# Performance work log

Measured on AMD Instinct MI355X. Metric: run time of the kernel, lower is better.

## Reference

```python
import jax, jax.numpy as jnp
import numpy as np

D_MODEL = 256
NUM_HEADS = 8
NUM_KV_HEADS = 4
HEAD_DIM = D_MODEL // NUM_HEADS
EPS = 1e-5


def layer_norm(x, g, b):
    mu = jnp.mean(x, axis=-1, keepdims=True)
    var = jnp.var(x, axis=-1, keepdims=True)
    return (x - mu) * jax.lax.rsqrt(var + EPS) * g + b


def gqa(x_q, x_kv, Wq, bq, Wk, bk, Wv, bv, Wo, bo):
    # x_q, x_kv: [BC, S, D]
    BC, S, D = x_q.shape
    G = NUM_HEADS // NUM_KV_HEADS
    q = (x_q @ Wq + bq).reshape(BC, S, NUM_HEADS, HEAD_DIM)
    k = (x_kv @ Wk + bk).reshape(BC, S, NUM_KV_HEADS, HEAD_DIM)
    v = (x_kv @ Wv + bv).reshape(BC, S, NUM_KV_HEADS, HEAD_DIM)
    # repeat_interleave over head dim to expand KV heads to query heads
    k = jnp.repeat(k, G, axis=2)
    v = jnp.repeat(v, G, axis=2)
    scale = 1.0 / np.sqrt(HEAD_DIM).astype(np.float32)
    scores = jnp.einsum('bqhd,bkhd->bhqk', q, k) * scale  # [BC,H,S,S]
    attn = jax.nn.softmax(scores, axis=-1)
    out = jnp.einsum('bhqk,bkhd->bqhd', attn, v).reshape(BC, S, D)
    return out @ Wo + bo


def _make_params(key):
    ks = jax.random.split(key, 20)
    D, Dkv = D_MODEL, NUM_KV_HEADS * HEAD_DIM
    s = 1.0 / np.sqrt(D).astype(np.float32)
    p = {}
    # 4 LayerNorms
    for name in ['spec_q', 'spec_kv', 'spat_q', 'spat_kv']:
        p[f'ln_{name}_g'] = jnp.ones((D,), jnp.float32)
        p[f'ln_{name}_b'] = jnp.zeros((D,), jnp.float32)
    # two GQA modules: s2t and t2s
    i = 0
    for tag in ['s2t', 't2s']:
        p[f'Wq_{tag}'] = jax.random.normal(ks[i], (D, D), jnp.float32) * s; i += 1
        p[f'bq_{tag}'] = jnp.zeros((D,), jnp.float32)
        p[f'Wk_{tag}'] = jax.random.normal(ks[i], (D, Dkv), jnp.float32) * s; i += 1
        p[f'bk_{tag}'] = jnp.zeros((Dkv,), jnp.float32)
        p[f'Wv_{tag}'] = jax.random.normal(ks[i], (D, Dkv), jnp.float32) * s; i += 1
        p[f'bv_{tag}'] = jnp.zeros((Dkv,), jnp.float32)
        p[f'Wo_{tag}'] = jax.random.normal(ks[i], (D, D), jnp.float32) * s; i += 1
        p[f'bo_{tag}'] = jnp.zeros((D,), jnp.float32)
    p['gate_spec'] = jnp.zeros((1,), jnp.float32)
    p['gate_spat'] = jnp.zeros((1,), jnp.float32)
    return p


def setup_inputs() -> dict:
    key = jax.random.key(0)
    k1, k2, k3 = jax.random.split(key, 3)
    B, S, C, D = 8, 64, 128, D_MODEL
    inp = {
        'x_spec': jax.random.normal(k1, (B, S, C, D), jnp.float32),
        'x_spat': jax.random.normal(k2, (B, S, C, D), jnp.float32),
    }
    inp.update(_make_params(k3))
    return inp


def reference(x_spec, x_spat,
              ln_spec_q_g, ln_spec_q_b, ln_spec_kv_g, ln_spec_kv_b,
              ln_spat_q_g, ln_spat_q_b, ln_spat_kv_g, ln_spat_kv_b,
              Wq_s2t, bq_s2t, Wk_s2t, bk_s2t, Wv_s2t, bv_s2t, Wo_s2t, bo_s2t,
              Wq_t2s, bq_t2s, Wk_t2s, bk_t2s, Wv_t2s, bv_t2s, Wo_t2s, bo_t2s,
              gate_spec, gate_spat):
    B, S, C, D = x_spec.shape
    # (B,S,C,D) -> (B*C, S, D)
    spec_flat = jnp.transpose(x_spec, (0, 2, 1, 3)).reshape(B * C, S, D)
    spat_flat = jnp.transpose(x_spat, (0, 2, 1, 3)).reshape(B * C, S, D)

    spec_q = layer_norm(spec_flat, ln_spec_q_g, ln_spec_q_b)
    spat_kv = layer_norm(spat_flat, ln_spat_kv_g, ln_spat_kv_b)
    delta_spec = gqa(spec_q, spat_kv, Wq_s2t, bq_s2t, Wk_s2t, bk_s2t, Wv_s2t, bv_s2t, Wo_s2t, bo_s2t)

    spat_q = layer_norm(spat_flat, ln_spat_q_g, ln_spat_q_b)
    spec_kv = layer_norm(spec_flat, ln_spec_kv_g, ln_spec_kv_b)
    delta_spat = gqa(spat_q, spec_kv, Wq_t2s, bq_t2s, Wk_t2s, bk_t2s, Wv_t2s, bv_t2s, Wo_t2s, bo_t2s)

    delta_spec = jnp.transpose(delta_spec.reshape(B, C, S, D), (0, 2, 1, 3))
    delta_spat = jnp.transpose(delta_spat.reshape(B, C, S, D), (0, 2, 1, 3))

    out_spec = x_spec + jax.nn.sigmoid(gate_spec) * delta_spec
    out_spat = x_spat + jax.nn.sigmoid(gate_spat) * delta_spat
    return (out_spec, out_spat)
```

## Files before the change

kernel.cpp:

```cpp
#include <hip/hip_runtime.h>

typedef short short8 __attribute__((ext_vector_type(8)));
typedef float f32x4 __attribute__((ext_vector_type(4)));

#define NELT 16777216

__device__ __forceinline__ float b2f(unsigned short u) {
    return __uint_as_float(((unsigned)u) << 16);
}
__device__ __forceinline__ unsigned short f2b(float f) {
    unsigned u = __float_as_uint(f);
    u += 0x7FFF + ((u >> 16) & 1);
    return (unsigned short)(u >> 16);
}
__device__ __forceinline__ void split2(float f, unsigned short& hi, unsigned short& lo) {
    unsigned short h = f2b(f);
    hi = h;
    lo = f2b(f - b2f(h));
}
__device__ __forceinline__ int xrow_off(int r) {
    int n = r >> 6, s = r & 63;
    int b = n >> 7, c = n & 127;
    return (((b << 6) + s) * 128 + c) << 8;
}
__device__ __forceinline__ int sw256(int row, int k) {
    return row * 256 + ((((k >> 3) ^ (row & 7)) << 3) | (k & 7));
}
__device__ __forceinline__ int boff(int nt, int kk, int ct, int lq, int lm) {
    return ((((nt * 8 + kk) * 4 + ct) * 4 + lq) * 16 + lm) * 16;
}

struct WArgs {
    const float* Wq[2]; const float* Wk[2]; const float* Wv[2]; const float* Wo[2];
    unsigned short* Bqkv[2]; unsigned short* Bo[2];
};
__global__ __launch_bounds__(256) void w_prep(WArgs A)
{
    const int dir = blockIdx.y;
    const int tid = blockIdx.x * 256 + threadIdx.x;
    const int lm = tid & 15, lq = (tid >> 4) & 3, ct = (tid >> 6) & 3;
    const int kk = (tid >> 8) & 7, nt = tid >> 11;
    const int c = ct * 16 + lm;
    {
        const float* W; int ldw, col;
        if (nt < 4)      { W = A.Wq[dir]; ldw = 256; col = nt * 64 + c; }
        else if (nt < 6) { W = A.Wk[dir]; ldw = 128; col = (nt - 4) * 64 + c; }
        else             { W = A.Wv[dir]; ldw = 128; col = (nt - 6) * 64 + c; }
        short8 h8, l8;
        #pragma unroll
        for (int j = 0; j < 8; ++j) {
            int k = kk * 32 + lq * 8 + j;
            unsigned short h, l;
            split2(W[k * ldw + col], h, l);
            h8[j] = (short)h; l8[j] = (short)l;
        }
        int off = boff(nt, kk, ct, lq, lm);
        *(short8*)&A.Bqkv[dir][off] = h8;
        *(short8*)&A.Bqkv[dir][off + 8] = l8;
    }
    if (nt < 4) {
        int col = nt * 64 + c;
        short8 h8, l8;
        #pragma unroll
        for (int j = 0; j < 8; ++j) {
            int k = kk * 32 + lq * 8 + j;
            unsigned short h, l;
            split2(A.Wo[dir][k * 256 + col], h, l);
            h8[j] = (short)h; l8[j] = (short)l;
        }
        int off = boff(nt, kk, ct, lq, lm);
        *(short8*)&A.Bo[dir][off] = h8;
        *(short8*)&A.Bo[dir][off + 8] = l8;
    }
}

struct FusedArgs {
    const float* xq[2];   const float* xkv[2];
    const float* gq[2];   const float* btq[2];
    const float* gkv[2];  const float* btkv[2];
    const unsigned short* Bqkv[2];
    const unsigned short* Bow[2];
    const float* bq[2];   const float* bk[2];
    const float* bv[2];   const float* bo[2];
    const float* gate[2];
    float* out[2];
};

__global__ __launch_bounds__(512, 4) void fused(FusedArgs P_)
{
    __shared__ char SM[71680];
    unsigned short* Ah = (unsigned short*)SM;
    unsigned short* Al = (unsigned short*)(SM + 16384);
    const int dir = blockIdx.y;
    const int n = blockIdx.x, t = threadIdx.x;
    const int r0 = n * 64;
    const int w = t >> 6, l = t & 63, lm = l & 15, lq = l >> 4;

    const float* xq  = P_.xq[dir];
    const float* xkv = P_.xkv[dir];
    const unsigned short* Bq  = P_.Bqkv[dir];
    const unsigned short* BoW = P_.Bow[dir];

    auto stage_half = [&](const float* X, const float4& gv, const float4& b4, int h) {
        float4 xv[4];
        #pragma unroll
        for (int it = 0; it < 4; ++it)
            xv[it] = *(const float4*)(X + xrow_off(r0 + h * 32 + it * 8 + w) + l * 4);
        #pragma unroll
        for (int it = 0; it < 4; ++it) {
            int row = it * 8 + w;
            float4 x4 = xv[it];
            float s1 = x4.x + x4.y + x4.z + x4.w;
            float s2 = x4.x * x4.x + x4.y * x4.y + x4.z * x4.z + x4.w * x4.w;
            #pragma unroll
            for (int m = 1; m < 64; m <<= 1) {
                s1 += __shfl_xor(s1, m);
                s2 += __shfl_xor(s2, m);
            }
            float mu = s1 * (1.f / 256.f);
            float rstd = rsqrtf(s2 * (1.f / 256.f) - mu * mu + 1e-5f);
            float v0 = (x4.x - mu) * rstd * gv.x + b4.x;
            float v1 = (x4.y - mu) * rstd * gv.y + b4.y;
            float v2 = (x4.z - mu) * rstd * gv.z + b4.z;
            float v3 = (x4.w - mu) * rstd * gv.w + b4.w;
            ushort4 oh, ol;
            split2(v0, oh.x, ol.x); split2(v1, oh.y, ol.y);
            split2(v2, oh.z, ol.z); split2(v3, oh.w, ol.w);
            *(ushort4*)&Ah[sw256(row, l * 4)] = oh;
            *(ushort4*)&Al[sw256(row, l * 4)] = ol;
        }
    };
    auto gemm_half = [&](f32x4 (&acc)[4][2], const unsigned short* B,
                         int nt, int ct0, int h) {
        #pragma unroll
        for (int kk = 0; kk < 8; ++kk) {
            int k0 = kk * 32 + lq * 8;
            short8 bh[2], bl[2];
            #pragma unroll
            for (int i = 0; i < 2; ++i) {
                int off = boff(nt, kk, ct0 + i, lq, lm);
                bh[i] = *(const short8*)&B[off];
                bl[i] = *(const short8*)&B[off + 8];
            }
            #pragma unroll
            for (int m2 = 0; m2 < 2; ++m2) {
                short8 ah = *(const short8*)&Ah[sw256(m2 * 16 + lm, k0)];
                short8 al = *(const short8*)&Al[sw256(m2 * 16 + lm, k0)];
                int m = 2 * h + m2;
                #pragma unroll
                for (int i = 0; i < 2; ++i) {
                    acc[m][i] = __builtin_amdgcn_mfma_f32_16x16x32_bf16(ah, bh[i], acc[m][i], 0, 0, 0);
                    acc[m][i] = __builtin_amdgcn_mfma_f32_16x16x32_bf16(al, bh[i], acc[m][i], 0, 0, 0);
                    acc[m][i] = __builtin_amdgcn_mfma_f32_16x16x32_bf16(ah, bl[i], acc[m][i], 0, 0, 0);
                }
            }
        }
    };

    {
        const float4 gv = *(const float4*)(P_.gkv[dir] + l * 4);
        const float4 b4 = *(const float4*)(P_.btkv[dir] + l * 4);
        f32x4 acc[4][2] = {};
        const int wk = w & 3;
        const bool isV = w >= 4;
        const int nt = (isV ? 6 : 4) + (wk >> 1);
        const int ct0 = (wk & 1) * 2;
        #pragma unroll
        for (int h = 0; h < 2; ++h) {
            stage_half(xkv, gv, b4, h);
            __syncthreads();
            gemm_half(acc, Bq, nt, ct0, h);
            __syncthreads();
        }
        const float* bias = isV ? P_.bv[dir] : P_.bk[dir];
        float bi0 = bias[wk * 32 + lm], bi1 = bias[wk * 32 + 16 + lm];
        if (!isV) {
            unsigned short* Ks = (unsigned short*)(SM + 32768 + wk * 5120);
            #pragma unroll
            for (int m = 0; m < 4; ++m)
                #pragma unroll
                for (int rg = 0; rg < 4; ++rg) {
                    int key = m * 16 + lq * 4 + rg;
                    Ks[key * 40 + lm]      = f2b(acc[m][0][rg] + bi0);
                    Ks[key * 40 + 16 + lm] = f2b(acc[m][1][rg] + bi1);
                }
        } else {
            unsigned short* Vs = (unsigned short*)(SM + 53248 + wk * 4608);
            #pragma unroll
            for (int m = 0; m < 4; ++m)
                #pragma unroll
                for (int rg = 0; rg < 4; ++rg) {
                    int key = m * 16 + lq * 4 + rg;
                    Vs[lm * 72 + key]        = f2b(acc[m][0][rg] + bi0);
                    Vs[(16 + lm) * 72 + key] = f2b(acc[m][1][rg] + bi1);
                }
        }
    }

    f32x4 o[4][2] = {};
    {
        const float4 gv = *(const float4*)(P_.gq[dir] + l * 4);
        const float4 b4 = *(const float4*)(P_.btq[dir] + l * 4);
        f32x4 qacc[4][2] = {};
        #pragma unroll
        for (int h = 0; h < 2; ++h) {
            stage_half(xq, gv, b4, h);
            __syncthreads();
            gemm_half(qacc, Bq, w >> 1, (w & 1) * 2, h);
            __syncthreads();
        }
        unsigned short* Qs = (unsigned short*)(SM + w * 4096);
        float bq0 = P_.bq[dir][w * 32 + lm], bq1 = P_.bq[dir][w * 32 + 16 + lm];
        #pragma unroll
        for (int m = 0; m < 4; ++m)
            #pragma unroll
            for (int rg = 0; rg < 4; ++rg) {
                int row = (m * 16 + lq * 4 + rg) * 32;
                Qs[row + lm]      = f2b(qacc[m][0][rg] + bq0);
                Qs[row + 16 + lm] = f2b(qacc[m][1][rg] + bq1);
            }
        const int g2 = w >> 1;
        short8 kf[4];
        {
            const unsigned short* Ks = (const unsigned short*)(SM + 32768 + g2 * 5120);
            #pragma unroll
            for (int nt = 0; nt < 4; ++nt)
                kf[nt] = *(const short8*)&Ks[(nt * 16 + lm) * 40 + lq * 8];
        }
        __syncthreads();
        short8 vb[2][2];
        {
            const unsigned short* Vs = (const unsigned short*)(SM + 53248 + g2 * 4608);
            #pragma unroll
            for (int kt = 0; kt < 2; ++kt) {
                vb[kt][0] = *(const short8*)&Vs[lm * 72 + kt * 32 + lq * 8];
                vb[kt][1] = *(const short8*)&Vs[(16 + lm) * 72 + kt * 32 + lq * 8];
            }
        }
        unsigned short* Ps = (unsigned short*)(SM + 32768 + w * 2304);
        const float scale = 0.17677669529663687f;
        #pragma unroll 1
        for (int mt = 0; mt < 4; ++mt) {
            short8 qf = *(const short8*)&Qs[(mt * 16 + lm) * 32 + lq * 8];
            f32x4 s[4];
            #pragma unroll
            for (int nt = 0; nt < 4; ++nt) {
                f32x4 z = {0, 0, 0, 0};
                s[nt] = __builtin_amdgcn_mfma_f32_16x16x32_bf16(qf, kf[nt], z, 0, 0, 0);
            }
            #pragma unroll
            for (int rg = 0; rg < 4; ++rg) {
                float mx = fmaxf(fmaxf(s[0][rg], s[1][rg]),
                                 fmaxf(s[2][rg], s[3][rg]));
                #pragma unroll
                for (int msk = 1; msk < 16; msk <<= 1)
                    mx = fmaxf(mx, __shfl_xor(mx, msk));
                float p0 = __expf((s[0][rg] - mx) * scale);
                float p1 = __expf((s[1][rg] - mx) * scale);
                float p2 = __expf((s[2][rg] - mx) * scale);
                float p3 = __expf((s[3][rg] - mx) * scale);
                float sum = p0 + p1 + p2 + p3;
                #pragma unroll
                for (int msk = 1; msk < 16; msk <<= 1)
                    sum += __shfl_xor(sum, msk);
                float inv = 1.f / sum;
                int rowb = (lq * 4 + rg) * 72 + lm;
                Ps[rowb + 0]  = f2b(p0 * inv);
                Ps[rowb + 16] = f2b(p1 * inv);
                Ps[rowb + 32] = f2b(p2 * inv);
                Ps[rowb + 48] = f2b(p3 * inv);
            }
            #pragma unroll
            for (int kt = 0; kt < 2; ++kt) {
                short8 pa = *(const short8*)&Ps[lm * 72 + kt * 32 + lq * 8];
                o[mt][0] = __builtin_amdgcn_mfma_f32_16x16x32_bf16(pa, vb[kt][0], o[mt][0], 0, 0, 0);
                o[mt][1] = __builtin_amdgcn_mfma_f32_16x16x32_bf16(pa, vb[kt][1], o[mt][1], 0, 0, 0);
            }
        }
    }
    __syncthreads();

    {
        f32x4 acc[4][2] = {};
        #pragma unroll
        for (int h = 0; h < 2; ++h) {
            #pragma unroll
            for (int m2 = 0; m2 < 2; ++m2) {
                int mt = 2 * h + m2;
                #pragma unroll
                for (int n2 = 0; n2 < 2; ++n2)
                    #pragma unroll
                    for (int rg = 0; rg < 4; ++rg) {
                        int row = m2 * 16 + lq * 4 + rg;
                        int col = w * 32 + n2 * 16 + lm;
                        unsigned short h_, l_;
                        split2(o[mt][n2][rg], h_, l_);
                        int sw = sw256(row, col);
                        Ah[sw] = h_;
                        Al[sw] = l_;
                    }
            }
            __syncthreads();
            gemm_half(acc, BoW, w >> 1, (w & 1) * 2, h);
            __syncthreads();
        }
        float sig = 1.f / (1.f + __expf(-P_.gate[dir][0]));
        const float* Xres = xq;
        float* Out = P_.out[dir];
        #pragma unroll
        for (int i = 0; i < 2; ++i) {
            int col = w * 32 + i * 16 + lm;
            float bias = P_.bo[dir][col];
            #pragma unroll
            for (int m = 0; m < 4; ++m)
                #pragma unroll
                for (int rg = 0; rg < 4; ++rg) {
                    int row = m * 16 + lq * 4 + rg;
                    int oidx = xrow_off(r0 + row) + col;
                    Out[oidx] = Xres[oidx] + sig * (acc[m][i][rg] + bias);
                }
        }
    }
}

extern "C" void kernel_launch(void* const* d_in, const int* in_sizes, int n_in,
                              void* d_out, int out_size, void* d_ws, size_t ws_size,
                              hipStream_t stream) {
    const float* x_spec = (const float*)d_in[0];
    const float* x_spat = (const float*)d_in[1];
    const float* ln_g[4] = {(const float*)d_in[2], (const float*)d_in[4],
                            (const float*)d_in[6], (const float*)d_in[8]};
    const float* ln_b[4] = {(const float*)d_in[3], (const float*)d_in[5],
                            (const float*)d_in[7], (const float*)d_in[9]};
    char* ws = (char*)d_ws;
    unsigned short* Bqkv[2] = {(unsigned short*)ws,
                               (unsigned short*)(ws + (512 << 10))};
    unsigned short* BoL[2]  = {(unsigned short*)(ws + (1024 << 10)),
                               (unsigned short*)(ws + (1280 << 10))};

    WArgs WA;
    for (int dir = 0; dir < 2; ++dir) {
        int base = 10 + dir * 8;
        WA.Wq[dir] = (const float*)d_in[base + 0];
        WA.Wk[dir] = (const float*)d_in[base + 2];
        WA.Wv[dir] = (const float*)d_in[base + 4];
        WA.Wo[dir] = (const float*)d_in[base + 6];
        WA.Bqkv[dir] = Bqkv[dir];
        WA.Bo[dir]   = BoL[dir];
    }
    w_prep<<<dim3(64, 2), 256, 0, stream>>>(WA);

    FusedArgs A;
    for (int dir = 0; dir < 2; ++dir) {
        int base = 10 + dir * 8;
        A.xq[dir]   = dir == 0 ? x_spec : x_spat;
        A.xkv[dir]  = dir == 0 ? x_spat : x_spec;
        A.gq[dir]   = dir == 0 ? ln_g[0] : ln_g[2];
        A.btq[dir]  = dir == 0 ? ln_b[0] : ln_b[2];
        A.gkv[dir]  = dir == 0 ? ln_g[3] : ln_g[1];
        A.btkv[dir] = dir == 0 ? ln_b[3] : ln_b[1];
        A.Bqkv[dir] = Bqkv[dir];
        A.Bow[dir]  = BoL[dir];
        A.bq[dir]   = (const float*)d_in[base + 1];
        A.bk[dir]   = (const float*)d_in[base + 3];
        A.bv[dir]   = (const float*)d_in[base + 5];
        A.bo[dir]   = (const float*)d_in[base + 7];
        A.gate[dir] = (const float*)d_in[26 + dir];
        A.out[dir]  = (float*)d_out + (size_t)dir * NELT;
    }
    fused<<<dim3(1024, 2), 512, 0, stream>>>(A);
}
```

Measured before the change: 473.3 us.

## Restructure LayerNorm row mapping, transpose score MFMA, single-pass output projection

LayerNorm staging now gives each 16-lane group one row, so the statistics reduction needs only 4 shuffle steps instead of 6 per row, and gamma/beta are read per segment. The score MFMA swaps its operands so each lane holds a full query column, which replaces the per-row 16-lane shuffle reductions with in-register max/sum plus two cross-group shuffles, and P is stored with vectorized writes. The output projection stages all 64 rows into shared memory at once and runs one full K loop, removing two of the four barriers there. The staged O buffer now spans 64KB of shared memory, and the operand swap changes the P layout, which must stay consistent with the PV MFMA read pattern.

```diff
diff --git a/kernel.cpp b/kernel.cpp
--- a/kernel.cpp
+++ b/kernel.cpp
@@ -101,24 +101,32 @@
     const unsigned short* Bq  = P_.Bqkv[dir];
     const unsigned short* BoW = P_.Bow[dir];
 
-    auto stage_half = [&](const float* X, const float4& gv, const float4& b4, int h) {
+    auto stage_half = [&](const float* X, const float* G, const float* BT, int h) {
+        const int lrow = w * 4 + lq;
+        const int xoff = xrow_off(r0 + h * 32 + lrow);
         float4 xv[4];
         #pragma unroll
-        for (int it = 0; it < 4; ++it)
-            xv[it] = *(const float4*)(X + xrow_off(r0 + h * 32 + it * 8 + w) + l * 4);
-        #pragma unroll
-        for (int it = 0; it < 4; ++it) {
-            int row = it * 8 + w;
-            float4 x4 = xv[it];
-            float s1 = x4.x + x4.y + x4.z + x4.w;
-            float s2 = x4.x * x4.x + x4.y * x4.y + x4.z * x4.z + x4.w * x4.w;
-            #pragma unroll
-            for (int m = 1; m < 64; m <<= 1) {
-                s1 += __shfl_xor(s1, m);
-                s2 += __shfl_xor(s2, m);
-            }
-            float mu = s1 * (1.f / 256.f);
-            float rstd = rsqrtf(s2 * (1.f / 256.f) - mu * mu + 1e-5f);
+        for (int seg = 0; seg < 4; ++seg)
+            xv[seg] = *(const float4*)(X + xoff + lm * 4 + seg * 64);
+        float s1 = 0.f, s2 = 0.f;
+        #pragma unroll
+        for (int seg = 0; seg < 4; ++seg) {
+            float4 x4 = xv[seg];
+            s1 += x4.x + x4.y + x4.z + x4.w;
+            s2 += x4.x * x4.x + x4.y * x4.y + x4.z * x4.z + x4.w * x4.w;
+        }
+        #pragma unroll
+        for (int m = 1; m < 16; m <<= 1) {
+            s1 += __shfl_xor(s1, m);
+            s2 += __shfl_xor(s2, m);
+        }
+        float mu = s1 * (1.f / 256.f);
+        float rstd = rsqrtf(s2 * (1.f / 256.f) - mu * mu + 1e-5f);
+        #pragma unroll
+        for (int seg = 0; seg < 4; ++seg) {
+            const float4 gv = *(const float4*)(G + lm * 4 + seg * 64);
+            const float4 b4 = *(const float4*)(BT + lm * 4 + seg * 64);
+            float4 x4 = xv[seg];
             float v0 = (x4.x - mu) * rstd * gv.x + b4.x;
             float v1 = (x4.y - mu) * rstd * gv.y + b4.y;
             float v2 = (x4.z - mu) * rstd * gv.z + b4.z;
@@ -126,8 +134,9 @@
             ushort4 oh, ol;
             split2(v0, oh.x, ol.x); split2(v1, oh.y, ol.y);
             split2(v2, oh.z, ol.z); split2(v3, oh.w, ol.w);
-            *(ushort4*)&Ah[sw256(row, l * 4)] = oh;
-            *(ushort4*)&Al[sw256(row, l * 4)] = ol;
+            int sw = sw256(lrow, lm * 4 + seg * 64);
+            *(ushort4*)&Ah[sw] = oh;
+            *(ushort4*)&Al[sw] = ol;
         }
     };
     auto gemm_half = [&](f32x4 (&acc)[4][2], const unsigned short* B,
@@ -158,8 +167,8 @@
     };
 
     {
-        const float4 gv = *(const float4*)(P_.gkv[dir] + l * 4);
-        const float4 b4 = *(const float4*)(P_.btkv[dir] + l * 4);
+        const float* G  = P_.gkv[dir];
+        const float* BT = P_.btkv[dir];
         f32x4 acc[4][2] = {};
         const int wk = w & 3;
         const bool isV = w >= 4;
@@ -167,7 +176,7 @@
         const int ct0 = (wk & 1) * 2;
         #pragma unroll
         for (int h = 0; h < 2; ++h) {
-            stage_half(xkv, gv, b4, h);
+            stage_half(xkv, G, BT, h);
             __syncthreads();
             gemm_half(acc, Bq, nt, ct0, h);
             __syncthreads();
@@ -199,12 +208,12 @@
 
     f32x4 o[4][2] = {};
     {
-        const float4 gv = *(const float4*)(P_.gq[dir] + l * 4);
-        const float4 b4 = *(const float4*)(P_.btq[dir] + l * 4);
+        const float* G  = P_.gq[dir];
+        const float* BT = P_.btq[dir];
         f32x4 qacc[4][2] = {};
         #pragma unroll
         for (int h = 0; h < 2; ++h) {
-            stage_half(xq, gv, b4, h);
+            stage_half(xq, G, BT, h);
             __syncthreads();
             gemm_half(qacc, Bq, w >> 1, (w & 1) * 2, h);
             __syncthreads();
@@ -246,29 +255,35 @@
             #pragma unroll
             for (int nt = 0; nt < 4; ++nt) {
                 f32x4 z = {0, 0, 0, 0};
-                s[nt] = __builtin_amdgcn_mfma_f32_16x16x32_bf16(qf, kf[nt], z, 0, 0, 0);
-            }
-            #pragma unroll
-            for (int rg = 0; rg < 4; ++rg) {
-                float mx = fmaxf(fmaxf(s[0][rg], s[1][rg]),
-                                 fmaxf(s[2][rg], s[3][rg]));
-                #pragma unroll
-                for (int msk = 1; msk < 16; msk <<= 1)
-                    mx = fmaxf(mx, __shfl_xor(mx, msk));
-                float p0 = __expf((s[0][rg] - mx) * scale);
-                float p1 = __expf((s[1][rg] - mx) * scale);
-                float p2 = __expf((s[2][rg] - mx) * scale);
-                float p3 = __expf((s[3][rg] - mx) * scale);
-                float sum = p0 + p1 + p2 + p3;
-                #pragma unroll
-                for (int msk = 1; msk < 16; msk <<= 1)
-                    sum += __shfl_xor(sum, msk);
-                float inv = 1.f / sum;
-                int rowb = (lq * 4 + rg) * 72 + lm;
-                Ps[rowb + 0]  = f2b(p0 * inv);
-                Ps[rowb + 16] = f2b(p1 * inv);
-                Ps[rowb + 32] = f2b(p2 * inv);
-                Ps[rowb + 48] = f2b(p3 * inv);
+                s[nt] = __builtin_amdgcn_mfma_f32_16x16x32_bf16(kf[nt], qf, z, 0, 0, 0);
+            }
+            float mx = s[0][0];
+            #pragma unroll
+            for (int nt = 0; nt < 4; ++nt)
+                #pragma unroll
+                for (int rg = 0; rg < 4; ++rg)
+                    mx = fmaxf(mx, s[nt][rg]);
+            mx = fmaxf(mx, __shfl_xor(mx, 16));
+            mx = fmaxf(mx, __shfl_xor(mx, 32));
+            float sum = 0.f;
+            #pragma unroll
+            for (int nt = 0; nt < 4; ++nt)
+                #pragma unroll
+                for (int rg = 0; rg < 4; ++rg) {
+                    s[nt][rg] = __expf((s[nt][rg] - mx) * scale);
+                    sum += s[nt][rg];
+                }
+            sum += __shfl_xor(sum, 16);
+            sum += __shfl_xor(sum, 32);
+            float inv = 1.f / sum;
+            #pragma unroll
+            for (int nt = 0; nt < 4; ++nt) {
+                ushort4 pw;
+                pw.x = f2b(s[nt][0] * inv);
+                pw.y = f2b(s[nt][1] * inv);
+                pw.z = f2b(s[nt][2] * inv);
+                pw.w = f2b(s[nt][3] * inv);
+                *(ushort4*)&Ps[lm * 72 + nt * 16 + lq * 4] = pw;
             }
             #pragma unroll
             for (int kt = 0; kt < 2; ++kt) {
@@ -281,28 +296,46 @@
     __syncthreads();
 
     {
+        unsigned short* AhF = (unsigned short*)SM;
+        unsigned short* AlF = (unsigned short*)(SM + 32768);
+        #pragma unroll
+        for (int mt = 0; mt < 4; ++mt)
+            #pragma unroll
+            for (int n2 = 0; n2 < 2; ++n2)
+                #pragma unroll
+                for (int rg = 0; rg < 4; ++rg) {
+                    int row = mt * 16 + lq * 4 + rg;
+                    int col = w * 32 + n2 * 16 + lm;
+                    unsigned short h_, l_;
+                    split2(o[mt][n2][rg], h_, l_);
+                    int sw = sw256(row, col);
+                    AhF[sw] = h_;
+                    AlF[sw] = l_;
+                }
+        __syncthreads();
         f32x4 acc[4][2] = {};
-        #pragma unroll
-        for (int h = 0; h < 2; ++h) {
-            #pragma unroll
-            for (int m2 = 0; m2 < 2; ++m2) {
-                int mt = 2 * h + m2;
-                #pragma unroll
-                for (int n2 = 0; n2 < 2; ++n2)
-                    #pragma unroll
-                    for (int rg = 0; rg < 4; ++rg) {
-                        int row = m2 * 16 + lq * 4 + rg;
-                        int col = w * 32 + n2 * 16 + lm;
-                        unsigned short h_, l_;
-                        split2(o[mt][n2][rg], h_, l_);
-                        int sw = sw256(row, col);
-                        Ah[sw] = h_;
-                        Al[sw] = l_;
-                    }
-            }
-            __syncthreads();
-            gemm_half(acc, BoW, w >> 1, (w & 1) * 2, h);
-            __syncthreads();
+        const int nt = w >> 1, ct0 = (w & 1) * 2;
+        #pragma unroll
+        for (int kk = 0; kk < 8; ++kk) {
+            int k0 = kk * 32 + lq * 8;
+            short8 bh[2], bl[2];
+            #pragma unroll
+            for (int i = 0; i < 2; ++i) {
+                int off = boff(nt, kk, ct0 + i, lq, lm);
+                bh[i] = *(const short8*)&BoW[off];
+                bl[i] = *(const short8*)&BoW[off + 8];
+            }
+            #pragma unroll
+            for (int m = 0; m < 4; ++m) {
+                short8 ah = *(const short8*)&AhF[sw256(m * 16 + lm, k0)];
+                short8 al = *(const short8*)&AlF[sw256(m * 16 + lm, k0)];
+                #pragma unroll
+                for (int i = 0; i < 2; ++i) {
+                    acc[m][i] = __builtin_amdgcn_mfma_f32_16x16x32_bf16(ah, bh[i], acc[m][i], 0, 0, 0);
+                    acc[m][i] = __builtin_amdgcn_mfma_f32_16x16x32_bf16(al, bh[i], acc[m][i], 0, 0, 0);
+                    acc[m][i] = __builtin_amdgcn_mfma_f32_16x16x32_bf16(ah, bl[i], acc[m][i], 0, 0, 0);
+                }
+            }
         }
         float sig = 1.f / (1.f + __expf(-P_.gate[dir][0]));
         const float* Xres = xq;
```

After: 456.1 us. 1.04x faster.
